# Kernel optimization log

Hardware: AMD Instinct MI355X
Metric: run time of the kernel (lower is better)

Reference implementation:

```python
import jax, jax.numpy as jnp
import numpy as np

B, S, H, NH, DH, FF = 8, 512, 768, 12, 64, 3072
EPS = 1e-3  # matches epsilon used in the repo's LayerNormalization


def layer_norm(x, g, b):
    mu = jnp.mean(x, axis=-1, keepdims=True)
    var = jnp.mean(jnp.square(x - mu), axis=-1, keepdims=True)
    return (x - mu) * jax.lax.rsqrt(var + EPS) * g + b


def setup_inputs() -> dict:
    key = jax.random.key(0)
    ks = jax.random.split(key, 12)
    init = lambda k, shp: (jax.random.normal(k, shp, dtype=jnp.float32) * 0.02)
    return {
        "hidden_states": jax.random.normal(ks[0], (B, S, H), dtype=jnp.float32),
        "attention_mask": jnp.ones((B, S), dtype=jnp.int32),
        "Wq": init(ks[1], (H, H)), "bq": jnp.zeros((H,), jnp.float32),
        "Wk": init(ks[2], (H, H)), "bk": jnp.zeros((H,), jnp.float32),
        "Wv": init(ks[3], (H, H)), "bv": jnp.zeros((H,), jnp.float32),
        "Wo": init(ks[4], (H, H)), "bo": jnp.zeros((H,), jnp.float32),
        "ln1_g": jnp.ones((H,), jnp.float32), "ln1_b": jnp.zeros((H,), jnp.float32),
        "W1": init(ks[5], (H, FF)), "b1": jnp.zeros((FF,), jnp.float32),
        "W2": init(ks[6], (FF, H)), "b2": jnp.zeros((H,), jnp.float32),
        "ln2_g": jnp.ones((H,), jnp.float32), "ln2_b": jnp.zeros((H,), jnp.float32),
    }


def reference(hidden_states, attention_mask, Wq, bq, Wk, bk, Wv, bv, Wo, bo,
              ln1_g, ln1_b, W1, b1, W2, b2, ln2_g, ln2_b):
    x = hidden_states  # [B,S,H]
    b, s, h = x.shape
    split = lambda t: t.reshape(b, s, NH, DH).transpose(0, 2, 1, 3)  # [B,NH,S,DH]
    q = split(x @ Wq + bq)
    k = split(x @ Wk + bk)
    v = split(x @ Wv + bv)
    scores = jnp.einsum("bhqd,bhkd->bhqk", q, k) / jnp.sqrt(jnp.float32(DH))
    # BERT-style additive mask: (1 - mask) * -10000, broadcast over heads/queries
    m = attention_mask.astype(jnp.float32)[:, None, None, :]
    scores = scores + (1.0 - m) * -10000.0
    probs = jax.nn.softmax(scores, axis=-1)
    ctx = jnp.einsum("bhqk,bhkd->bhqd", probs, v)
    ctx = ctx.transpose(0, 2, 1, 3).reshape(b, s, h)  # [B,S,H]
    attn_out = ctx @ Wo + bo
    h1 = layer_norm(attn_out + x, ln1_g, ln1_b)
    ff = jax.nn.gelu(h1 @ W1 + b1, approximate=False) @ W2 + b2
    return layer_norm(ff + h1, ln2_g, ln2_b)
```

## Files before the change

kernel.cpp:

```cpp
#include <hip/hip_runtime.h>
#include <hip/hip_bf16.h>

#define H_DIM 768
#define FF_DIM 3072
#define NHEAD 12
#define DHEAD 64
#define SEQ 512
#define TOK 4096

typedef __bf16 bf16;
using bf16x8 = __attribute__((ext_vector_type(8))) __bf16;
using f32x4  = __attribute__((ext_vector_type(4))) float;

static __device__ __forceinline__ f32x4 mfma16(bf16x8 a, bf16x8 b, f32x4 c) {
  return __builtin_amdgcn_mfma_f32_16x16x32_bf16(a, b, c, 0, 0, 0);
}

__global__ __launch_bounds__(256) void cvt_k(const float* __restrict__ in, bf16* __restrict__ out, int n) {
  int i = (blockIdx.x * 256 + threadIdx.x) * 8;
  if (i >= n) return;
  float4 a = *(const float4*)(in + i);
  float4 b = *(const float4*)(in + i + 4);
  bf16x8 o;
  o[0] = (bf16)a.x; o[1] = (bf16)a.y; o[2] = (bf16)a.z; o[3] = (bf16)a.w;
  o[4] = (bf16)b.x; o[5] = (bf16)b.y; o[6] = (bf16)b.z; o[7] = (bf16)b.w;
  *(bf16x8*)(out + i) = o;
}

__global__ __launch_bounds__(256) void cvtT_k(const float* __restrict__ in, bf16* __restrict__ out,
                                              int R, int C) {
  __shared__ bf16 tile[32][33];
  int c0 = blockIdx.x * 32, r0 = blockIdx.y * 32;
  int tx = threadIdx.x & 31, ty = threadIdx.x >> 5;
  for (int i = 0; i < 32; i += 8) tile[ty + i][tx] = (bf16)in[(size_t)(r0 + ty + i) * C + c0 + tx];
  __syncthreads();
  for (int i = 0; i < 32; i += 8) out[(size_t)(c0 + ty + i) * R + r0 + tx] = tile[tx][ty + i];
}

struct GemmArgs {
  const bf16* A;
  const bf16* W[3];
  const float* bias[3];
  bf16* outB[3];
  float* outF[3];
  const float* resF[3];
  int M, N, K, act;
};

#define BK 32
#define LPAD 40

template <int BM, int BN, int MI, int NI>
__global__ __launch_bounds__(256) void gemm_t(GemmArgs args) {
  __shared__ bf16 As[BM][LPAD];
  __shared__ bf16 Bs[BN][LPAD];
  int z = blockIdx.z;
  const bf16* A  = args.A;
  const bf16* Bt = args.W[z];
  int Kd = args.K, N = args.N;
  int m0 = blockIdx.y * BM, n0 = blockIdx.x * BN;
  int t = threadIdx.x;
  int wid = t >> 6, lane = t & 63, quad = lane >> 4, l16 = lane & 15;
  int wm = wid >> 1, wn = wid & 1;

  f32x4 zero4 = {0.0f, 0.0f, 0.0f, 0.0f};
  f32x4 acc[MI][NI];
#pragma unroll
  for (int mi = 0; mi < MI; mi++)
#pragma unroll
    for (int ni = 0; ni < NI; ni++) acc[mi][ni] = zero4;

  constexpr int APT = BM * BK / 256;
  constexpr int BPT = BN * BK / 256;
  int arow, acol, brow, bcol;
  if constexpr (APT == 16) { arow = t >> 1; acol = (t & 1) * 16; }
  else                     { arow = t >> 2; acol = (t & 3) * 8; }
  if constexpr (BPT == 16) { brow = t >> 1; bcol = (t & 1) * 16; }
  else                     { brow = t >> 2; bcol = (t & 3) * 8; }
  const bf16* gA = A  + (size_t)(m0 + arow) * Kd + acol;
  const bf16* gB = Bt + (size_t)(n0 + brow) * Kd + bcol;

  for (int k0 = 0; k0 < Kd; k0 += BK) {
    bf16x8 a0, a1, b0, b1;
    a0 = *(const bf16x8*)(gA + k0);
    if constexpr (APT == 16) a1 = *(const bf16x8*)(gA + k0 + 8);
    b0 = *(const bf16x8*)(gB + k0);
    if constexpr (BPT == 16) b1 = *(const bf16x8*)(gB + k0 + 8);
    __syncthreads();
    *(bf16x8*)&As[arow][acol] = a0;
    if constexpr (APT == 16) *(bf16x8*)&As[arow][acol + 8] = a1;
    *(bf16x8*)&Bs[brow][bcol] = b0;
    if constexpr (BPT == 16) *(bf16x8*)&Bs[brow][bcol + 8] = b1;
    __syncthreads();
    bf16x8 af[MI], bfr[NI];
#pragma unroll
    for (int mi = 0; mi < MI; mi++) af[mi] = *(const bf16x8*)&As[wm * (MI * 16) + mi * 16 + l16][quad * 8];
#pragma unroll
    for (int ni = 0; ni < NI; ni++) bfr[ni] = *(const bf16x8*)&Bs[wn * (NI * 16) + ni * 16 + l16][quad * 8];
#pragma unroll
    for (int mi = 0; mi < MI; mi++)
#pragma unroll
      for (int ni = 0; ni < NI; ni++) acc[mi][ni] = mfma16(af[mi], bfr[ni], acc[mi][ni]);
  }

  const float* bias = args.bias[z];
  bf16* outB = args.outB[z];
  float* outF = args.outF[z];
  const float* resF = args.resF[z];
  float bv[NI];
#pragma unroll
  for (int ni = 0; ni < NI; ni++) bv[ni] = bias[n0 + wn * (NI * 16) + ni * 16 + l16];
#pragma unroll
  for (int mi = 0; mi < MI; mi++) {
#pragma unroll
    for (int r = 0; r < 4; r++) {
      int row = m0 + wm * (MI * 16) + mi * 16 + quad * 4 + r;
#pragma unroll
      for (int ni = 0; ni < NI; ni++) {
        int col = n0 + wn * (NI * 16) + ni * 16 + l16;
        float v = acc[mi][ni][r] + bv[ni];
        if (args.act) v = 0.5f * v * (1.0f + erff(v * 0.70710678118654752f));
        size_t idx = (size_t)row * N + col;
        if (resF) v += resF[idx];
        if (outB) outB[idx] = (bf16)v;
        if (outF) outF[idx] = v;
      }
    }
  }
}

#define CHK 128
__global__ __launch_bounds__(256) void attn_k(const bf16* __restrict__ Qg, const bf16* __restrict__ Kg,
                                              const bf16* __restrict__ Vg, const int* __restrict__ mask,
                                              bf16* __restrict__ ctx) {
  __shared__ bf16 Ks[CHK][72];
  __shared__ bf16 Vts[DHEAD][CHK + 8];
  __shared__ float maskadd[CHK];
  __shared__ bf16 Ps[4][16][LPAD];
  int bh = blockIdx.y;
  int b = bh / NHEAD, h = bh % NHEAD;
  int q0 = blockIdx.x * 64;
  int t = threadIdx.x;
  int wid = t >> 6, lane = t & 63, quad = lane >> 4, l16 = lane & 15;
  size_t base = (size_t)b * SEQ * H_DIM + (size_t)h * DHEAD;

  int qrow = q0 + wid * 16 + l16;
  bf16x8 qf0 = *(const bf16x8*)(Qg + base + (size_t)qrow * H_DIM + quad * 8);
  bf16x8 qf1 = *(const bf16x8*)(Qg + base + (size_t)qrow * H_DIM + 32 + quad * 8);

  f32x4 zero4 = {0.0f, 0.0f, 0.0f, 0.0f};
  f32x4 o[4];
  float m_i[4], l_i[4];
#pragma unroll
  for (int r = 0; r < 4; r++) { o[r] = zero4; m_i[r] = -1e30f; l_i[r] = 0.0f; }

  for (int c0 = 0; c0 < SEQ; c0 += CHK) {
    __syncthreads();
    {
      int row = t >> 1, half = (t & 1) * 32;
      const bf16* g = Kg + base + (size_t)(c0 + row) * H_DIM + half;
      *(bf16x8*)&Ks[row][half]      = *(const bf16x8*)g;
      *(bf16x8*)&Ks[row][half + 8]  = *(const bf16x8*)(g + 8);
      *(bf16x8*)&Ks[row][half + 16] = *(const bf16x8*)(g + 16);
      *(bf16x8*)&Ks[row][half + 24] = *(const bf16x8*)(g + 24);
    }
#pragma unroll
    for (int pass = 0; pass < 4; ++pass) {
      int s = (t >> 3) + pass * 32, dg = (t & 7) * 8;
      bf16x8 v = *(const bf16x8*)(Vg + base + (size_t)(c0 + s) * H_DIM + dg);
#pragma unroll
      for (int j = 0; j < 8; j++) Vts[dg + j][s] = v[j];
    }
    if (t < CHK) maskadd[t] = (1.0f - (float)mask[b * SEQ + c0 + t]) * -10000.0f;
    __syncthreads();

    for (int kt = 0; kt < CHK; kt += 32) {
      f32x4 s0 = zero4, s1 = zero4;
      bf16x8 k0a = *(const bf16x8*)&Ks[kt + l16][quad * 8];
      bf16x8 k0b = *(const bf16x8*)&Ks[kt + l16][32 + quad * 8];
      bf16x8 k1a = *(const bf16x8*)&Ks[kt + 16 + l16][quad * 8];
      bf16x8 k1b = *(const bf16x8*)&Ks[kt + 16 + l16][32 + quad * 8];
      s0 = mfma16(qf0, k0a, s0); s0 = mfma16(qf1, k0b, s0);
      s1 = mfma16(qf0, k1a, s1); s1 = mfma16(qf1, k1b, s1);
      float add0 = maskadd[kt + l16], add1 = maskadd[kt + 16 + l16];
#pragma unroll
      for (int r = 0; r < 4; r++) {
        float v0 = s0[r] * 0.125f + add0;
        float v1 = s1[r] * 0.125f + add1;
        float mx = fmaxf(v0, v1);
#pragma unroll
        for (int off = 1; off < 16; off <<= 1) mx = fmaxf(mx, __shfl_xor(mx, off));
        float mnew = fmaxf(m_i[r], mx);
        float p0 = __expf(v0 - mnew), p1 = __expf(v1 - mnew);
        float alpha = __expf(m_i[r] - mnew);
        m_i[r] = mnew;
        float ps = p0 + p1;
#pragma unroll
        for (int off = 1; off < 16; off <<= 1) ps += __shfl_xor(ps, off);
        l_i[r] = l_i[r] * alpha + ps;
#pragma unroll
        for (int ni = 0; ni < 4; ni++) o[ni][r] *= alpha;
        Ps[wid][quad * 4 + r][l16]      = (bf16)p0;
        Ps[wid][quad * 4 + r][16 + l16] = (bf16)p1;
      }
      bf16x8 pa = *(const bf16x8*)&Ps[wid][l16][quad * 8];
#pragma unroll
      for (int ni = 0; ni < 4; ni++) {
        bf16x8 vb = *(const bf16x8*)&Vts[ni * 16 + l16][kt + quad * 8];
        o[ni] = mfma16(pa, vb, o[ni]);
      }
    }
  }
#pragma unroll
  for (int r = 0; r < 4; r++) {
    int row = q0 + wid * 16 + quad * 4 + r;
    float inv = 1.0f / l_i[r];
#pragma unroll
    for (int ni = 0; ni < 4; ni++)
      ctx[base + (size_t)row * H_DIM + ni * 16 + l16] = (bf16)(o[ni][r] * inv);
  }
}

__global__ __launch_bounds__(256) void ln_k(const float* __restrict__ in, const float* __restrict__ g,
                                            const float* __restrict__ bta, bf16* __restrict__ outB,
                                            float* __restrict__ outF) {
  int row = blockIdx.x, t = threadIdx.x;
  const float* x = in + (size_t)row * H_DIM;
  float v[3], s = 0.0f, sq = 0.0f;
#pragma unroll
  for (int i = 0; i < 3; i++) { v[i] = x[t + i * 256]; s += v[i]; sq += v[i] * v[i]; }
#pragma unroll
  for (int off = 32; off >= 1; off >>= 1) { s += __shfl_down(s, off); sq += __shfl_down(sq, off); }
  __shared__ float ssum[4], ssq[4], smu, srs;
  int lane = t & 63, w = t >> 6;
  if (lane == 0) { ssum[w] = s; ssq[w] = sq; }
  __syncthreads();
  if (t == 0) {
    float S = ssum[0] + ssum[1] + ssum[2] + ssum[3];
    float Q = ssq[0] + ssq[1] + ssq[2] + ssq[3];
    float mu = S * (1.0f / H_DIM);
    float var = Q * (1.0f / H_DIM) - mu * mu;
    smu = mu;
    srs = rsqrtf(var + 1e-3f);
  }
  __syncthreads();
  float mu = smu, rs = srs;
#pragma unroll
  for (int i = 0; i < 3; i++) {
    int c = t + i * 256;
    float y = (v[i] - mu) * rs * g[c] + bta[c];
    if (outB) outB[(size_t)row * H_DIM + c] = (bf16)y;
    if (outF) outF[(size_t)row * H_DIM + c] = y;
  }
}

extern "C" void kernel_launch(void* const* d_in, const int* in_sizes, int n_in,
                              void* d_out, int out_size, void* d_ws, size_t ws_size,
                              hipStream_t stream) {
  const float* x    = (const float*)d_in[0];
  const int*   mask = (const int*)d_in[1];
  const float* Wq = (const float*)d_in[2];  const float* bq = (const float*)d_in[3];
  const float* Wk = (const float*)d_in[4];  const float* bk = (const float*)d_in[5];
  const float* Wv = (const float*)d_in[6];  const float* bv = (const float*)d_in[7];
  const float* Wo = (const float*)d_in[8];  const float* bo = (const float*)d_in[9];
  const float* ln1g = (const float*)d_in[10]; const float* ln1b = (const float*)d_in[11];
  const float* W1 = (const float*)d_in[12]; const float* b1 = (const float*)d_in[13];
  const float* W2 = (const float*)d_in[14]; const float* b2 = (const float*)d_in[15];
  const float* ln2g = (const float*)d_in[16]; const float* ln2b = (const float*)d_in[17];
  float* out = (float*)d_out;
  (void)ws_size; (void)in_sizes; (void)n_in; (void)out_size;

  char* w = (char*)d_ws;
  const size_t SZ_TH  = (size_t)TOK * H_DIM * 2;
  const size_t SZ_W   = (size_t)H_DIM * H_DIM * 2;
  const size_t SZ_WF  = (size_t)H_DIM * FF_DIM * 2;
  bf16* xB  = (bf16*)(w);
  bf16* WqT = (bf16*)(w + SZ_TH);
  bf16* WkT = (bf16*)(w + SZ_TH + SZ_W);
  bf16* WvT = (bf16*)(w + SZ_TH + 2 * SZ_W);
  bf16* WoT = (bf16*)(w + SZ_TH + 3 * SZ_W);
  bf16* W1T = (bf16*)(w + SZ_TH + 4 * SZ_W);
  bf16* W2T = (bf16*)(w + SZ_TH + 4 * SZ_W + SZ_WF);
  char* pQ  = w + SZ_TH + 4 * SZ_W + 2 * SZ_WF;
  bf16* QB  = (bf16*)(pQ);
  bf16* KB  = (bf16*)(pQ + SZ_TH);
  bf16* VB  = (bf16*)(pQ + 2 * SZ_TH);
  bf16* CTX = (bf16*)(pQ + 3 * SZ_TH);
  float* PRE1 = (float*)(pQ + 4 * SZ_TH);
  bf16* H1   = QB;
  float* H1F = (float*)(pQ + SZ_TH);
  bf16* FFA  = CTX;
  float* PRE2 = (float*)(w);

  dim3 tb(256);

  cvt_k<<<(TOK * H_DIM) / 2048, tb, 0, stream>>>(x, xB, TOK * H_DIM);
  cvtT_k<<<dim3(24, 24), tb, 0, stream>>>(Wq, WqT, H_DIM, H_DIM);
  cvtT_k<<<dim3(24, 24), tb, 0, stream>>>(Wk, WkT, H_DIM, H_DIM);
  cvtT_k<<<dim3(24, 24), tb, 0, stream>>>(Wv, WvT, H_DIM, H_DIM);
  cvtT_k<<<dim3(24, 24), tb, 0, stream>>>(Wo, WoT, H_DIM, H_DIM);
  cvtT_k<<<dim3(96, 24), tb, 0, stream>>>(W1, W1T, H_DIM, FF_DIM);
  cvtT_k<<<dim3(24, 96), tb, 0, stream>>>(W2, W2T, FF_DIM, H_DIM);

  GemmArgs ga = {};
  ga.A = xB; ga.M = TOK; ga.N = H_DIM; ga.K = H_DIM; ga.act = 0;
  ga.W[0] = WqT; ga.W[1] = WkT; ga.W[2] = WvT;
  ga.bias[0] = bq; ga.bias[1] = bk; ga.bias[2] = bv;
  ga.outB[0] = QB; ga.outB[1] = KB; ga.outB[2] = VB;
  gemm_t<128, 128, 4, 4><<<dim3(H_DIM / 128, TOK / 128, 3), tb, 0, stream>>>(ga);

  attn_k<<<dim3(SEQ / 64, 8 * NHEAD), tb, 0, stream>>>(QB, KB, VB, mask, CTX);

  GemmArgs go = {};
  go.A = CTX; go.M = TOK; go.N = H_DIM; go.K = H_DIM; go.act = 0;
  go.W[0] = WoT; go.bias[0] = bo; go.resF[0] = x; go.outF[0] = PRE1;
  gemm_t<64, 64, 2, 2><<<dim3(H_DIM / 64, TOK / 64, 1), tb, 0, stream>>>(go);

  ln_k<<<TOK, tb, 0, stream>>>(PRE1, ln1g, ln1b, H1, H1F);

  GemmArgs g1 = {};
  g1.A = H1; g1.M = TOK; g1.N = FF_DIM; g1.K = H_DIM; g1.act = 1;
  g1.W[0] = W1T; g1.bias[0] = b1; g1.outB[0] = FFA;
  gemm_t<128, 128, 4, 4><<<dim3(FF_DIM / 128, TOK / 128, 1), tb, 0, stream>>>(g1);

  GemmArgs g2 = {};
  g2.A = FFA; g2.M = TOK; g2.N = H_DIM; g2.K = FF_DIM; g2.act = 0;
  g2.W[0] = W2T; g2.bias[0] = b2; g2.resF[0] = H1F; g2.outF[0] = PRE2;
  gemm_t<64, 64, 2, 2><<<dim3(H_DIM / 64, TOK / 64, 1), tb, 0, stream>>>(g2);

  ln_k<<<TOK, tb, 0, stream>>>(PRE2, ln2g, ln2b, nullptr, out);
}
```

Measured before the change: 335.3 us.

## Use direct global-to-LDS loads in GEMMs and split-K with atomics for N=768

Replaces the register-staged GEMM tile loads with global_load_lds direct-to-LDS transfers, using an unpadded LDS layout. The two N=768 projection GEMMs move from 64x64 tiles to 128x128 tiles split four ways along K. Each slice accumulates into a float buffer with atomicAdd, and that buffer is pre-filled with residual plus bias by a new init kernel. The aim is to cut load instruction overhead and to raise tile efficiency while keeping enough blocks in flight. The cost is the extra init pass, atomic traffic and possible LDS bank conflicts from the unpadded layout.

```diff
diff --git a/kernel.cpp b/kernel.cpp
--- a/kernel.cpp
+++ b/kernel.cpp
@@ -14,6 +14,11 @@
 
 static __device__ __forceinline__ f32x4 mfma16(bf16x8 a, bf16x8 b, f32x4 c) {
   return __builtin_amdgcn_mfma_f32_16x16x32_bf16(a, b, c, 0, 0, 0);
+}
+
+static __device__ __forceinline__ void gl2lds16(const bf16* g, bf16* l) {
+  __builtin_amdgcn_global_load_lds((const __attribute__((address_space(1))) void*)g,
+                                   (__attribute__((address_space(3))) void*)l, 16, 0, 0);
 }
 
 __global__ __launch_bounds__(256) void cvt_k(const float* __restrict__ in, bf16* __restrict__ out, int n) {
@@ -37,99 +42,126 @@
   for (int i = 0; i < 32; i += 8) out[(size_t)(c0 + ty + i) * R + r0 + tx] = tile[tx][ty + i];
 }
 
+__global__ __launch_bounds__(256) void initres_k(const float* __restrict__ res,
+                                                 const float* __restrict__ bias,
+                                                 float* __restrict__ out, int total4, int n4) {
+  int i = blockIdx.x * 256 + threadIdx.x;
+  if (i >= total4) return;
+  float4 r = ((const float4*)res)[i];
+  const float* bp = bias + (i % n4) * 4;
+  float4 o = {r.x + bp[0], r.y + bp[1], r.z + bp[2], r.w + bp[3]};
+  ((float4*)out)[i] = o;
+}
+
 struct GemmArgs {
   const bf16* A;
   const bf16* W[3];
   const float* bias[3];
   bf16* outB[3];
-  float* outF[3];
-  const float* resF[3];
-  int M, N, K, act;
+  float* outF;
+  int M, N, K, kSlices;
 };
 
 #define BK 32
-#define LPAD 40
-
-template <int BM, int BN, int MI, int NI>
-__global__ __launch_bounds__(256) void gemm_t(GemmArgs args) {
-  __shared__ bf16 As[BM][LPAD];
-  __shared__ bf16 Bs[BN][LPAD];
+
+template <int MODE>
+__global__ __launch_bounds__(256) void gemm_gl(GemmArgs args) {
+  __shared__ bf16 As[128 * BK];
+  __shared__ bf16 Bs[128 * BK];
   int z = blockIdx.z;
-  const bf16* A  = args.A;
-  const bf16* Bt = args.W[z];
+  const bf16* A = args.A;
+  const bf16* Bt;
   int Kd = args.K, N = args.N;
-  int m0 = blockIdx.y * BM, n0 = blockIdx.x * BN;
+  int kBeg, kEnd;
+  if constexpr (MODE == 2) {
+    Bt = args.W[0];
+    int ks = Kd / args.kSlices;
+    kBeg = z * ks; kEnd = kBeg + ks;
+  } else {
+    Bt = args.W[z];
+    kBeg = 0; kEnd = Kd;
+  }
+  int m0 = blockIdx.y * 128, n0 = blockIdx.x * 128;
   int t = threadIdx.x;
   int wid = t >> 6, lane = t & 63, quad = lane >> 4, l16 = lane & 15;
   int wm = wid >> 1, wn = wid & 1;
 
   f32x4 zero4 = {0.0f, 0.0f, 0.0f, 0.0f};
-  f32x4 acc[MI][NI];
-#pragma unroll
-  for (int mi = 0; mi < MI; mi++)
-#pragma unroll
-    for (int ni = 0; ni < NI; ni++) acc[mi][ni] = zero4;
-
-  constexpr int APT = BM * BK / 256;
-  constexpr int BPT = BN * BK / 256;
-  int arow, acol, brow, bcol;
-  if constexpr (APT == 16) { arow = t >> 1; acol = (t & 1) * 16; }
-  else                     { arow = t >> 2; acol = (t & 3) * 8; }
-  if constexpr (BPT == 16) { brow = t >> 1; bcol = (t & 1) * 16; }
-  else                     { brow = t >> 2; bcol = (t & 3) * 8; }
-  const bf16* gA = A  + (size_t)(m0 + arow) * Kd + acol;
-  const bf16* gB = Bt + (size_t)(n0 + brow) * Kd + bcol;
-
-  for (int k0 = 0; k0 < Kd; k0 += BK) {
-    bf16x8 a0, a1, b0, b1;
-    a0 = *(const bf16x8*)(gA + k0);
-    if constexpr (APT == 16) a1 = *(const bf16x8*)(gA + k0 + 8);
-    b0 = *(const bf16x8*)(gB + k0);
-    if constexpr (BPT == 16) b1 = *(const bf16x8*)(gB + k0 + 8);
+  f32x4 acc[4][4];
+#pragma unroll
+  for (int mi = 0; mi < 4; mi++)
+#pragma unroll
+    for (int ni = 0; ni < 4; ni++) acc[mi][ni] = zero4;
+
+  int ch = wid * 2;
+  int rA = lane >> 2;
+  int cE = (lane & 3) * 8;
+  const bf16* gA0 = A  + (size_t)(m0 + ch * 16 + rA) * Kd + cE;
+  const bf16* gA1 = gA0 + (size_t)16 * Kd;
+  const bf16* gB0 = Bt + (size_t)(n0 + ch * 16 + rA) * Kd + cE;
+  const bf16* gB1 = gB0 + (size_t)16 * Kd;
+  bf16* lA0 = As + ch * 512;
+  bf16* lA1 = As + ch * 512 + 512;
+  bf16* lB0 = Bs + ch * 512;
+  bf16* lB1 = Bs + ch * 512 + 512;
+
+  for (int k0 = kBeg; k0 < kEnd; k0 += BK) {
     __syncthreads();
-    *(bf16x8*)&As[arow][acol] = a0;
-    if constexpr (APT == 16) *(bf16x8*)&As[arow][acol + 8] = a1;
-    *(bf16x8*)&Bs[brow][bcol] = b0;
-    if constexpr (BPT == 16) *(bf16x8*)&Bs[brow][bcol + 8] = b1;
+    gl2lds16(gA0 + k0, lA0);
+    gl2lds16(gA1 + k0, lA1);
+    gl2lds16(gB0 + k0, lB0);
+    gl2lds16(gB1 + k0, lB1);
     __syncthreads();
-    bf16x8 af[MI], bfr[NI];
-#pragma unroll
-    for (int mi = 0; mi < MI; mi++) af[mi] = *(const bf16x8*)&As[wm * (MI * 16) + mi * 16 + l16][quad * 8];
-#pragma unroll
-    for (int ni = 0; ni < NI; ni++) bfr[ni] = *(const bf16x8*)&Bs[wn * (NI * 16) + ni * 16 + l16][quad * 8];
-#pragma unroll
-    for (int mi = 0; mi < MI; mi++)
-#pragma unroll
-      for (int ni = 0; ni < NI; ni++) acc[mi][ni] = mfma16(af[mi], bfr[ni], acc[mi][ni]);
-  }
-
-  const float* bias = args.bias[z];
-  bf16* outB = args.outB[z];
-  float* outF = args.outF[z];
-  const float* resF = args.resF[z];
-  float bv[NI];
-#pragma unroll
-  for (int ni = 0; ni < NI; ni++) bv[ni] = bias[n0 + wn * (NI * 16) + ni * 16 + l16];
-#pragma unroll
-  for (int mi = 0; mi < MI; mi++) {
-#pragma unroll
-    for (int r = 0; r < 4; r++) {
-      int row = m0 + wm * (MI * 16) + mi * 16 + quad * 4 + r;
-#pragma unroll
-      for (int ni = 0; ni < NI; ni++) {
-        int col = n0 + wn * (NI * 16) + ni * 16 + l16;
-        float v = acc[mi][ni][r] + bv[ni];
-        if (args.act) v = 0.5f * v * (1.0f + erff(v * 0.70710678118654752f));
-        size_t idx = (size_t)row * N + col;
-        if (resF) v += resF[idx];
-        if (outB) outB[idx] = (bf16)v;
-        if (outF) outF[idx] = v;
+    bf16x8 af[4], bfr[4];
+#pragma unroll
+    for (int mi = 0; mi < 4; mi++) af[mi] = *(const bf16x8*)&As[(wm * 64 + mi * 16 + l16) * BK + quad * 8];
+#pragma unroll
+    for (int ni = 0; ni < 4; ni++) bfr[ni] = *(const bf16x8*)&Bs[(wn * 64 + ni * 16 + l16) * BK + quad * 8];
+#pragma unroll
+    for (int mi = 0; mi < 4; mi++)
+#pragma unroll
+      for (int ni = 0; ni < 4; ni++) acc[mi][ni] = mfma16(af[mi], bfr[ni], acc[mi][ni]);
+  }
+
+  if constexpr (MODE == 2) {
+    float* outF = args.outF;
+#pragma unroll
+    for (int mi = 0; mi < 4; mi++) {
+#pragma unroll
+      for (int r = 0; r < 4; r++) {
+        int row = m0 + wm * 64 + mi * 16 + quad * 4 + r;
+#pragma unroll
+        for (int ni = 0; ni < 4; ni++) {
+          int col = n0 + wn * 64 + ni * 16 + l16;
+          atomicAdd(&outF[(size_t)row * N + col], acc[mi][ni][r]);
+        }
       }
     }
+  } else {
+    const float* bias = args.bias[z];
+    bf16* outB = args.outB[z];
+    float bv[4];
+#pragma unroll
+    for (int ni = 0; ni < 4; ni++) bv[ni] = bias[n0 + wn * 64 + ni * 16 + l16];
+#pragma unroll
+    for (int mi = 0; mi < 4; mi++) {
+#pragma unroll
+      for (int r = 0; r < 4; r++) {
+        int row = m0 + wm * 64 + mi * 16 + quad * 4 + r;
+#pragma unroll
+        for (int ni = 0; ni < 4; ni++) {
+          int col = n0 + wn * 64 + ni * 16 + l16;
+          float v = acc[mi][ni][r] + bv[ni];
+          if constexpr (MODE == 1) v = 0.5f * v * (1.0f + erff(v * 0.70710678118654752f));
+          outB[(size_t)row * N + col] = (bf16)v;
+        }
+      }
+    }
   }
 }
 
 #define CHK 128
+#define LPAD 40
 __global__ __launch_bounds__(256) void attn_k(const bf16* __restrict__ Qg, const bf16* __restrict__ Kg,
                                               const bf16* __restrict__ Vg, const int* __restrict__ mask,
                                               bf16* __restrict__ ctx) {
@@ -303,30 +335,30 @@
   cvtT_k<<<dim3(24, 96), tb, 0, stream>>>(W2, W2T, FF_DIM, H_DIM);
 
   GemmArgs ga = {};
-  ga.A = xB; ga.M = TOK; ga.N = H_DIM; ga.K = H_DIM; ga.act = 0;
+  ga.A = xB; ga.M = TOK; ga.N = H_DIM; ga.K = H_DIM; ga.kSlices = 1;
   ga.W[0] = WqT; ga.W[1] = WkT; ga.W[2] = WvT;
   ga.bias[0] = bq; ga.bias[1] = bk; ga.bias[2] = bv;
   ga.outB[0] = QB; ga.outB[1] = KB; ga.outB[2] = VB;
-  gemm_t<128, 128, 4, 4><<<dim3(H_DIM / 128, TOK / 128, 3), tb, 0, stream>>>(ga);
+  gemm_gl<0><<<dim3(H_DIM / 128, TOK / 128, 3), tb, 0, stream>>>(ga);
 
   attn_k<<<dim3(SEQ / 64, 8 * NHEAD), tb, 0, stream>>>(QB, KB, VB, mask, CTX);
 
+  initres_k<<<(TOK * H_DIM / 4 + 255) / 256, tb, 0, stream>>>(x, bo, PRE1, TOK * H_DIM / 4, H_DIM / 4);
   GemmArgs go = {};
-  go.A = CTX; go.M = TOK; go.N = H_DIM; go.K = H_DIM; go.act = 0;
-  go.W[0] = WoT; go.bias[0] = bo; go.resF[0] = x; go.outF[0] = PRE1;
-  gemm_t<64, 64, 2, 2><<<dim3(H_DIM / 64, TOK / 64, 1), tb, 0, stream>>>(go);
-
+  go.A = CTX; go.M = TOK; go.N = H_DIM; go.K = H_DIM; go.kSlices = 4;
+  go.W[0] = WoT; go.outF = PRE1;
+  gemm_gl<2><<<dim3(H_DIM / 128, TOK / 128, 4), tb, 0, stream>>>(go);
   ln_k<<<TOK, tb, 0, stream>>>(PRE1, ln1g, ln1b, H1, H1F);
 
   GemmArgs g1 = {};
-  g1.A = H1; g1.M = TOK; g1.N = FF_DIM; g1.K = H_DIM; g1.act = 1;
+  g1.A = H1; g1.M = TOK; g1.N = FF_DIM; g1.K = H_DIM; g1.kSlices = 1;
   g1.W[0] = W1T; g1.bias[0] = b1; g1.outB[0] = FFA;
-  gemm_t<128, 128, 4, 4><<<dim3(FF_DIM / 128, TOK / 128, 1), tb, 0, stream>>>(g1);
-
+  gemm_gl<1><<<dim3(FF_DIM / 128, TOK / 128, 1), tb, 0, stream>>>(g1);
+
+  initres_k<<<(TOK * H_DIM / 4 + 255) / 256, tb, 0, stream>>>(H1F, b2, PRE2, TOK * H_DIM / 4, H_DIM / 4);
   GemmArgs g2 = {};
-  g2.A = FFA; g2.M = TOK; g2.N = H_DIM; g2.K = FF_DIM; g2.act = 0;
-  g2.W[0] = W2T; g2.bias[0] = b2; g2.resF[0] = H1F; g2.outF[0] = PRE2;
-  gemm_t<64, 64, 2, 2><<<dim3(H_DIM / 64, TOK / 64, 1), tb, 0, stream>>>(g2);
-
+  g2.A = FFA; g2.M = TOK; g2.N = H_DIM; g2.K = FF_DIM; g2.kSlices = 4;
+  g2.W[0] = W2T; g2.outF = PRE2;
+  gemm_gl<2><<<dim3(H_DIM / 128, TOK / 128, 4), tb, 0, stream>>>(g2);
   ln_k<<<TOK, tb, 0, stream>>>(PRE2, ln2g, ln2b, nullptr, out);
 }
```

Measured after the change: 368.4 us. 9.9% more time.
